# Kernel optimization log

Hardware: AMD Instinct MI355X
Metric: run time of the kernel (lower is better)

## Reference

```python
import jax, jax.numpy as jnp
import numpy as np

GRID_H = 128
GRID_W = 128
N_POS = 8192
RAD = 1.5
EPS = 1e-12


def setup_inputs() -> dict:
    key = jax.random.key(0)
    k_pos, k_maze = jax.random.split(key)
    # positions uniformly spread over the maze extent [0, H] x [0, W]
    pos = jax.random.uniform(k_pos, (N_POS, 2), dtype=jnp.float32)
    pos = pos * jnp.array([GRID_H, GRID_W], dtype=jnp.float32)
    maze = (jax.random.uniform(k_maze, (GRID_H, GRID_W)) < 0.3).astype(jnp.float32)
    rad = jnp.float32(RAD)
    return {"pos": pos, "maze": maze, "rad": rad}


def reference(pos, maze, rad):
    # pos:  [N, 2] query positions
    # maze: [H, W] occupancy grid (1.0 = wall cell)
    # rad:  scalar collision radius
    H, W = maze.shape
    # cell centers at (i + 0.5, j + 0.5)
    ii = jnp.arange(H, dtype=pos.dtype) + 0.5
    jj = jnp.arange(W, dtype=pos.dtype) + 0.5
    ci, cj = jnp.meshgrid(ii, jj, indexing="ij")
    centers = jnp.stack([ci.ravel(), cj.ravel()], axis=-1)  # [M, 2], M = H*W
    occ = maze.ravel()                                       # [M]
    # squared distances via ||p||^2 + ||c||^2 - 2 p.c  (avoids [N, M, 2] diff tensor)
    p2 = jnp.sum(pos * pos, axis=-1, keepdims=True)          # [N, 1]
    c2 = jnp.sum(centers * centers, axis=-1)                 # [M]
    d2 = p2 + c2 - 2.0 * jnp.einsum("nd,md->nm", pos, centers)  # [N, M]
    d = jnp.sqrt(jnp.maximum(d2, EPS))
    # penetration penalty within collision radius, weighted by occupancy
    pen = jax.nn.relu(rad - d) * occ                         # [N, M]
    count = jnp.sum(pen)
    return count
```

## Files before the change

kernel.cpp:

```cpp
#include <hip/hip_runtime.h>

#define GRID_H 128
#define GRID_W 128
#define N_POS  8192
#define EPS_F  1e-12f

__global__ __launch_bounds__(256) void MazeCollision_kernel(
    const float* __restrict__ pos,
    const float* __restrict__ maze,
    const float* __restrict__ rad_p,
    float* __restrict__ out)
{
    const float rad = rad_p[0];
    const int tid = blockIdx.x * blockDim.x + threadIdx.x;

    float acc = 0.0f;
    if (tid < N_POS) {
        const float x = pos[2 * tid + 0];
        const float y = pos[2 * tid + 1];
        int ilo = max(0, (int)floorf(x - 0.5f - rad));
        int ihi = min(GRID_H - 1, (int)ceilf(x - 0.5f + rad));
        int jlo = max(0, (int)floorf(y - 0.5f - rad));
        int jhi = min(GRID_W - 1, (int)ceilf(y - 0.5f + rad));
        for (int i = ilo; i <= ihi; ++i) {
            const float dx = x - ((float)i + 0.5f);
            const float dx2 = dx * dx;
            const int rowbase = i * GRID_W;
            for (int j = jlo; j <= jhi; ++j) {
                const float dy = y - ((float)j + 0.5f);
                const float d2 = dx2 + dy * dy;
                const float d = sqrtf(fmaxf(d2, EPS_F));
                const float pen = fmaxf(rad - d, 0.0f);
                acc += pen * maze[rowbase + j];
            }
        }
    }

    #pragma unroll
    for (int off = 32; off > 0; off >>= 1)
        acc += __shfl_down(acc, off, 64);

    __shared__ float wave_sums[4];
    const int lane = threadIdx.x & 63;
    const int wave = threadIdx.x >> 6;
    if (lane == 0) wave_sums[wave] = acc;
    __syncthreads();

    if (threadIdx.x == 0) {
        const float s = wave_sums[0] + wave_sums[1] + wave_sums[2] + wave_sums[3];
        atomicAdd(out, s);
    }
}

extern "C" void kernel_launch(void* const* d_in, const int* in_sizes, int n_in,
                              void* d_out, int out_size, void* d_ws, size_t ws_size,
                              hipStream_t stream) {
    const float* pos  = (const float*)d_in[0];
    const float* maze = (const float*)d_in[1];
    const float* rad  = (const float*)d_in[2];
    float* out = (float*)d_out;

    hipMemsetAsync(out, 0, (size_t)out_size * sizeof(float), stream);

    const int block = 256;
    const int grid = (N_POS + block - 1) / block;
    MazeCollision_kernel<<<grid, block, 0, stream>>>(pos, maze, rad, out);
}
```

Before: 14.50 us.

## Run collision sum in a single block with maze staged in LDS

Collapses the launch to one 1024-thread block that copies the 64KB maze into shared memory and loops over all 8192 positions, eight per thread. The final value is written directly, which removes the memset launch and the atomic accumulation. In exchange all work runs on a single CU, so the cost of the per-position neighbourhood loops (about 16 cells each) is serialised there rather than spread across many CUs.

New measurement: 41.85 us. 189% more time.

```diff
diff --git a/kernel.cpp b/kernel.cpp
--- a/kernel.cpp
+++ b/kernel.cpp
@@ -3,35 +3,46 @@
 #define GRID_H 128
 #define GRID_W 128
 #define N_POS  8192
+#define NTHREADS 1024
 #define EPS_F  1e-12f
 
-__global__ __launch_bounds__(256) void MazeCollision_kernel(
+__global__ __launch_bounds__(NTHREADS) void MazeCollision_kernel(
     const float* __restrict__ pos,
     const float* __restrict__ maze,
     const float* __restrict__ rad_p,
     float* __restrict__ out)
 {
+    __shared__ float smaze[GRID_H * GRID_W];
+    const int t = threadIdx.x;
+
+    {
+        const float4* m4 = (const float4*)maze;
+        float4* s4 = (float4*)smaze;
+        #pragma unroll
+        for (int k = 0; k < (GRID_H * GRID_W / 4) / NTHREADS; ++k)
+            s4[t + k * NTHREADS] = m4[t + k * NTHREADS];
+    }
     const float rad = rad_p[0];
-    const int tid = blockIdx.x * blockDim.x + threadIdx.x;
+    __syncthreads();
 
     float acc = 0.0f;
-    if (tid < N_POS) {
-        const float x = pos[2 * tid + 0];
-        const float y = pos[2 * tid + 1];
-        int ilo = max(0, (int)floorf(x - 0.5f - rad));
-        int ihi = min(GRID_H - 1, (int)ceilf(x - 0.5f + rad));
-        int jlo = max(0, (int)floorf(y - 0.5f - rad));
-        int jhi = min(GRID_W - 1, (int)ceilf(y - 0.5f + rad));
+    const float2* p2 = (const float2*)pos;
+    #pragma unroll
+    for (int k = 0; k < N_POS / NTHREADS; ++k) {
+        const float2 xy = p2[t + k * NTHREADS];
+        const float x = xy.x, y = xy.y;
+        const int ilo = max(0, (int)floorf(x - 0.5f - rad));
+        const int ihi = min(GRID_H - 1, (int)ceilf(x - 0.5f + rad));
+        const int jlo = max(0, (int)floorf(y - 0.5f - rad));
+        const int jhi = min(GRID_W - 1, (int)ceilf(y - 0.5f + rad));
         for (int i = ilo; i <= ihi; ++i) {
             const float dx = x - ((float)i + 0.5f);
             const float dx2 = dx * dx;
-            const int rowbase = i * GRID_W;
+            const float* row = &smaze[i * GRID_W];
             for (int j = jlo; j <= jhi; ++j) {
                 const float dy = y - ((float)j + 0.5f);
-                const float d2 = dx2 + dy * dy;
-                const float d = sqrtf(fmaxf(d2, EPS_F));
-                const float pen = fmaxf(rad - d, 0.0f);
-                acc += pen * maze[rowbase + j];
+                const float d = sqrtf(fmaxf(dx2 + dy * dy, EPS_F));
+                acc += fmaxf(rad - d, 0.0f) * row[j];
             }
         }
     }
@@ -40,15 +51,17 @@
     for (int off = 32; off > 0; off >>= 1)
         acc += __shfl_down(acc, off, 64);
 
-    __shared__ float wave_sums[4];
-    const int lane = threadIdx.x & 63;
-    const int wave = threadIdx.x >> 6;
-    if (lane == 0) wave_sums[wave] = acc;
+    __shared__ float wsum[NTHREADS / 64];
+    const int lane = t & 63, wave = t >> 6;
+    if (lane == 0) wsum[wave] = acc;
     __syncthreads();
 
-    if (threadIdx.x == 0) {
-        const float s = wave_sums[0] + wave_sums[1] + wave_sums[2] + wave_sums[3];
-        atomicAdd(out, s);
+    if (t < 16) {
+        float v = wsum[t];
+        #pragma unroll
+        for (int off = 8; off > 0; off >>= 1)
+            v += __shfl_down(v, off, 64);
+        if (t == 0) out[0] = v;
     }
 }
 
@@ -60,9 +73,5 @@
     const float* rad  = (const float*)d_in[2];
     float* out = (float*)d_out;
 
-    hipMemsetAsync(out, 0, (size_t)out_size * sizeof(float), stream);
-
-    const int block = 256;
-    const int grid = (N_POS + block - 1) / block;
-    MazeCollision_kernel<<<grid, block, 0, stream>>>(pos, maze, rad, out);
+    MazeCollision_kernel<<<1, NTHREADS, 0, stream>>>(pos, maze, rad, out);
 }
```
